# Optimization experiments

Hardware: AMD Instinct MI355X
Metric: run time of the kernel (lower is better)

Reference implementation:

```python
import jax, jax.numpy as jnp
import numpy as np
import math

B, S, D, H = 2, 2048, 1024, 16
DK = D // H


def setup_inputs() -> dict:
    key = jax.random.key(0)
    ks = jax.random.split(key, 11)
    s = 1.0 / math.sqrt(D)
    return {
        "q": jax.random.normal(ks[0], (B, S, D), jnp.float32),
        "k": jax.random.normal(ks[1], (B, S, D), jnp.float32),
        "v": jax.random.normal(ks[2], (B, S, D), jnp.float32),
        "Wq": jax.random.normal(ks[3], (D, D), jnp.float32) * s,
        "bq": jax.random.normal(ks[4], (D,), jnp.float32) * s,
        "Wk": jax.random.normal(ks[5], (D, D), jnp.float32) * s,
        "bk": jax.random.normal(ks[6], (D,), jnp.float32) * s,
        "Wv": jax.random.normal(ks[7], (D, D), jnp.float32) * s,
        "bv": jax.random.normal(ks[8], (D,), jnp.float32) * s,
        "Wo": jax.random.normal(ks[9], (D, D), jnp.float32) * s,
        "bo": jax.random.normal(ks[10], (D,), jnp.float32) * s,
    }


def reference(q, k, v, Wq, bq, Wk, bk, Wv, bv, Wo, bo):
    bs = q.shape[0]
    # linear projections, split heads: [B, H, S, DK]
    qh = (q @ Wq.T + bq).reshape(bs, -1, H, DK).transpose(0, 2, 1, 3)
    kh = (k @ Wk.T + bk).reshape(bs, -1, H, DK).transpose(0, 2, 1, 3)
    vh = (v @ Wv.T + bv).reshape(bs, -1, H, DK).transpose(0, 2, 1, 3)
    # scaled dot-product attention (dropout in eval mode -> identity)
    scores = jnp.einsum('bhqd,bhkd->bhqk', qh, kh) / math.sqrt(DK)
    attn = jax.nn.softmax(scores, axis=-1)
    out = jnp.einsum('bhqk,bhkd->bhqd', attn, vh)
    concat = out.transpose(0, 2, 1, 3).reshape(bs, -1, D)
    return concat @ Wo.T + bo
```

## Files before the change

kernel.cpp:

```cpp
#include <hip/hip_runtime.h>
#include <stdint.h>

#define DEV __device__ __forceinline__

typedef __bf16 bf16;
typedef __bf16 bf16x8 __attribute__((ext_vector_type(8)));
typedef unsigned short u16x8 __attribute__((ext_vector_type(8)));
typedef float f32x4 __attribute__((ext_vector_type(4)));
typedef uint32_t u32x4 __attribute__((ext_vector_type(4)));

static constexpr int S = 2048, D = 1024, NH = 16;
static constexpr float QSCALE = 0.125f * 1.44269504088896340736f;
static constexpr float DTHR = 8.0f;

union BU { u16x8 u; bf16x8 v; };
union PU { u32x4 u; bf16x8 v; };

DEV uint32_t pack2(float a, float b) {
  union { __bf16 h; uint16_t u; } x, y;
  x.h = (__bf16)a; y.h = (__bf16)b;
  return (uint32_t)x.u | ((uint32_t)y.u << 16);
}

struct CvtArgs { const float* s[7]; bf16* d[7]; };
__global__ __launch_bounds__(256) void cvt_all(CvtArgs a) {
  int blk = blockIdx.x, seg, rel;
  if (blk < 6144) { seg = blk >> 11; rel = blk & 2047; }
  else { int bb = blk - 6144; seg = 3 + (bb >> 9); rel = bb & 511; }
  int i = rel * 256 + threadIdx.x;
  const float4* p = (const float4*)a.s[seg] + (size_t)i * 2;
  float4 x = p[0], y = p[1];
  bf16x8 o;
  o[0] = (bf16)x.x; o[1] = (bf16)x.y; o[2] = (bf16)x.z; o[3] = (bf16)x.w;
  o[4] = (bf16)y.x; o[5] = (bf16)y.y; o[6] = (bf16)y.z; o[7] = (bf16)y.w;
  ((bf16x8*)a.d[seg])[i] = o;
}

DEV void async_copy16(bf16* lds_dst, const bf16* g_src) {
  __builtin_amdgcn_global_load_lds(
      (const __attribute__((address_space(1))) void*)(g_src),
      (__attribute__((address_space(3))) void*)(lds_dst),
      16, 0, 0);
}

struct GArgs {
  const bf16* A[3]; const bf16* W[3]; const float* bias[3];
  bf16* Cb[3]; float* Cf[3]; float scale[3];
};

template <bool OUT_F32>
__global__ __launch_bounds__(256, 2)
void gemm_multi(GArgs g) {
  constexpr int N = 1024, K = 1024;
  const int z = blockIdx.z;
  const bf16* A = g.A[z];
  const bf16* Bt = g.W[z];
  const float* bias = g.bias[z];
  const float scale = g.scale[z];

  __shared__ bf16 As[128 * 32];
  __shared__ bf16 Bs[64 * 32];
  const int t = threadIdx.x;
  const int w = t >> 6, l = t & 63;
  const int lr = l & 15, lg = l >> 4;
  const int m0 = blockIdx.y * 128, n0 = blockIdx.x * 64;

  f32x4 acc[2][4] = {};

  const int srow = t >> 2, scol = (t & 3) * 8;
  const bf16* Aptr = A + (size_t)(m0 + srow) * K + scol;
  const bf16* Bptr = Bt + (size_t)(n0 + srow) * K + scol;
  bf16* AsDst = &As[w * 512];
  bf16* BsDst = &Bs[w * 512];

  for (int k0 = 0; k0 < K; k0 += 32) {
    async_copy16(AsDst,        Aptr + k0);
    async_copy16(AsDst + 2048, Aptr + (size_t)64 * K + k0);
    async_copy16(BsDst,        Bptr + k0);
    __syncthreads();
    bf16x8 af[2], bfr[4];
#pragma unroll
    for (int i = 0; i < 2; i++)
      af[i] = *(const bf16x8*)&As[(w * 32 + i * 16 + lr) * 32 + lg * 8];
#pragma unroll
    for (int n = 0; n < 4; n++)
      bfr[n] = *(const bf16x8*)&Bs[(n * 16 + lr) * 32 + lg * 8];
#pragma unroll
    for (int mi = 0; mi < 2; mi++)
#pragma unroll
      for (int ni = 0; ni < 4; ni++)
        acc[mi][ni] = __builtin_amdgcn_mfma_f32_16x16x32_bf16(
            af[mi], bfr[ni], acc[mi][ni], 0, 0, 0);
    __syncthreads();
  }

#pragma unroll
  for (int mi = 0; mi < 2; mi++) {
#pragma unroll
    for (int ni = 0; ni < 4; ni++) {
      int col = n0 + ni * 16 + lr;
      float bv = bias[col];
#pragma unroll
      for (int r = 0; r < 4; r++) {
        int row = m0 + w * 32 + mi * 16 + lg * 4 + r;
        float v = (acc[mi][ni][r] + bv) * scale;
        if (OUT_F32) g.Cf[z][(size_t)row * N + col] = v;
        else         g.Cb[z][(size_t)row * N + col] = (bf16)v;
      }
    }
  }
}

__global__ __launch_bounds__(256, 2)
void attn_kernel(const bf16* __restrict__ Qp, const bf16* __restrict__ Kp,
                 const bf16* __restrict__ Vp, bf16* __restrict__ Oc) {
  __shared__ uint4 ldsu[2048];
  char* lds = (char*)ldsu;

  const int t = threadIdx.x, w = t >> 6, l = t & 63;
  const int lr = l & 15, lg = l >> 4;
  const int bh = blockIdx.y, b = bh >> 4, h = bh & 15;
  const int q0 = blockIdx.x * 128;
  const size_t base = (size_t)b * S * D + (size_t)h * 64;
  const size_t TILE = (size_t)64 * D;

  bf16x8 qf[2][2];
  {
    const bf16* qb = Qp + base + (size_t)(q0 + w * 32 + lr) * D + lg * 8;
#pragma unroll
    for (int qs = 0; qs < 2; qs++)
#pragma unroll
      for (int ks = 0; ks < 2; ks++)
        qf[qs][ks] = *(const bf16x8*)(qb + (size_t)qs * 16 * D + ks * 32);
  }

  f32x4 accO[2][4] = {};
  float mrun[2] = {-1e30f, -1e30f}, lsum[2] = {0.f, 0.f};

  const bf16* kptr[2];
#pragma unroll
  for (int c = 0; c < 2; c++) {
    int o = w * 2048 + c * 1024 + l * 16;
    int rho = o >> 7;
    int seg16 = ((o & 127) ^ ((rho & 7) << 4)) >> 4;
    int mm = rho >> 4;
    int srow = ((mm & 1) << 5) | (((rho >> 2) & 3) << 3) | ((mm >> 1) << 2) | (rho & 3);
    kptr[c] = Kp + base + (size_t)srow * D + seg16 * 8;
  }

  const int vu = t & 31, vc = t >> 5;
  const bf16* Vg = Vp + base + (size_t)(2 * vu) * D + vc * 8;
  int vwa[8];
#pragma unroll
  for (int j = 0; j < 8; j++)
    vwa[j] = 16384 + (((vc * 8 + j) * 128 + vu * 4) ^ (j << 4));

  const int rswz = (lr & 7) << 4;

  async_copy16((bf16*)(lds + w * 2048),        kptr[0]);
  async_copy16((bf16*)(lds + w * 2048 + 1024), kptr[1]);
  u16x8 va = *(const u16x8*)(Vg);
  u16x8 vb = *(const u16x8*)(Vg + D);
  __syncthreads();
  {
#pragma unroll
    for (int j = 0; j < 8; j++) {
      uint32_t dw = (uint32_t)va[j] | ((uint32_t)vb[j] << 16);
      *(uint32_t*)(lds + vwa[j]) = dw;
    }
  }
  va = *(const u16x8*)(Vg + TILE);
  vb = *(const u16x8*)(Vg + TILE + D);
  __syncthreads();

  const bf16* kp0 = kptr[0] + TILE;
  const bf16* kp1 = kptr[1] + TILE;
  const bf16* vg2 = Vg + 2 * TILE;

  for (int it = 0; it < 32; ++it) {
    const int cur = (it & 1) * 8192;
    const int nxt = ((it + 1) & 1) * 8192;
    const bool hasN = it < 31, hasN2 = it < 30;

    if (hasN) {
      async_copy16((bf16*)(lds + nxt + w * 2048),        kp0);
      async_copy16((bf16*)(lds + nxt + w * 2048 + 1024), kp1);
      kp0 += TILE; kp1 += TILE;
    }
    const bf16* pv = hasN2 ? vg2 : (Vp + base);
    u16x8 ta = *(const u16x8*)(pv);
    u16x8 tb = *(const u16x8*)(pv + D);
    vg2 += TILE;

    f32x4 sc[2][4] = {};
#pragma unroll
    for (int ks = 0; ks < 2; ks++) {
      BU kf[4];
#pragma unroll
      for (int m = 0; m < 4; m++)
        kf[m].u = *(const u16x8*)(lds + cur +
                   ((((m * 16 + lr) * 128) + ks * 64 + lg * 16) ^ rswz));
      __builtin_amdgcn_s_setprio(1);
#pragma unroll
      for (int m = 0; m < 4; m++)
#pragma unroll
        for (int qs = 0; qs < 2; qs++)
          sc[qs][m] = __builtin_amdgcn_mfma_f32_16x16x32_bf16(
              kf[m].v, qf[qs][ks], sc[qs][m], 0, 0, 0);
      __builtin_amdgcn_s_setprio(0);
    }

    float mx[2];
#pragma unroll
    for (int qs = 0; qs < 2; qs++) {
      float a0 = fmaxf(fmaxf(sc[qs][0][0], sc[qs][0][1]), fmaxf(sc[qs][0][2], sc[qs][0][3]));
      float a1 = fmaxf(fmaxf(sc[qs][1][0], sc[qs][1][1]), fmaxf(sc[qs][1][2], sc[qs][1][3]));
      float a2 = fmaxf(fmaxf(sc[qs][2][0], sc[qs][2][1]), fmaxf(sc[qs][2][2], sc[qs][2][3]));
      float a3 = fmaxf(fmaxf(sc[qs][3][0], sc[qs][3][1]), fmaxf(sc[qs][3][2], sc[qs][3][3]));
      mx[qs] = fmaxf(fmaxf(a0, a1), fmaxf(a2, a3));
    }
    bool stable = (mx[0] <= mrun[0] + DTHR) & (mx[1] <= mrun[1] + DTHR);
    if (!__all(stable)) {
      float alq[2];
#pragma unroll
      for (int qs = 0; qs < 2; qs++) {
        float m2 = fmaxf(mx[qs], __shfl_xor(mx[qs], 16));
        m2 = fmaxf(m2, __shfl_xor(m2, 32));
        float mn = fmaxf(mrun[qs], m2);
        float al = exp2f(mrun[qs] - mn);
        mrun[qs] = mn;
        lsum[qs] *= al;
        alq[qs] = al;
      }
#pragma unroll
      for (int qs = 0; qs < 2; qs++)
#pragma unroll
        for (int r = 0; r < 4; r++) {
          float a = __shfl(alq[qs], (lg << 4) | (lg * 4 + r));
#pragma unroll
          for (int n = 0; n < 4; n++) accO[qs][n][r] *= a;
        }
    }
    uint32_t pk[2][4][2];
#pragma unroll
    for (int qs = 0; qs < 2; qs++) {
      float s = 0.f;
#pragma unroll
      for (int m = 0; m < 4; m++) {
        float p0 = exp2f(sc[qs][m][0] - mrun[qs]);
        float p1 = exp2f(sc[qs][m][1] - mrun[qs]);
        float p2 = exp2f(sc[qs][m][2] - mrun[qs]);
        float p3 = exp2f(sc[qs][m][3] - mrun[qs]);
        s += (p0 + p1) + (p2 + p3);
        pk[qs][m][0] = pack2(p0, p1);
        pk[qs][m][1] = pack2(p2, p3);
      }
      lsum[qs] += s;
    }

    if (hasN) {
#pragma unroll
      for (int j = 0; j < 8; j++) {
        uint32_t dw = (uint32_t)va[j] | ((uint32_t)vb[j] << 16);
        *(uint32_t*)(lds + vwa[j] + nxt) = dw;
      }
    }

#pragma unroll
    for (int ks = 0; ks < 2; ks++) {
      PU pa[2];
#pragma unroll
      for (int qs = 0; qs < 2; qs++) {
        pa[qs].u[0] = pk[qs][ks][0];
        pa[qs].u[1] = pk[qs][ks][1];
        pa[qs].u[2] = pk[qs][2 + ks][0];
        pa[qs].u[3] = pk[qs][2 + ks][1];
      }
      BU vf[4];
#pragma unroll
      for (int n = 0; n < 4; n++)
        vf[n].u = *(const u16x8*)(lds + 16384 + cur +
                   ((((n * 16 + lr) * 128) + ks * 64 + lg * 16) ^ rswz));
      __builtin_amdgcn_s_setprio(1);
#pragma unroll
      for (int n = 0; n < 4; n++)
#pragma unroll
        for (int qs = 0; qs < 2; qs++)
          accO[qs][n] = __builtin_amdgcn_mfma_f32_16x16x32_bf16(
              pa[qs].v, vf[n].v, accO[qs][n], 0, 0, 0);
      __builtin_amdgcn_s_setprio(0);
    }

    va = ta; vb = tb;
    __syncthreads();
  }

#pragma unroll
  for (int qs = 0; qs < 2; qs++) {
    lsum[qs] += __shfl_xor(lsum[qs], 16);
    lsum[qs] += __shfl_xor(lsum[qs], 32);
  }
#pragma unroll
  for (int qs = 0; qs < 2; qs++)
#pragma unroll
    for (int r = 0; r < 4; r++) {
      float lv = __shfl(lsum[qs], (lg << 4) | (lg * 4 + r));
      float rl = 1.0f / lv;
      int row = q0 + w * 32 + qs * 16 + lg * 4 + r;
      bf16* orow = Oc + base + (size_t)row * D;
#pragma unroll
      for (int n = 0; n < 4; n++) orow[n * 16 + lr] = (bf16)(accO[qs][n][r] * rl);
    }
}

extern "C" void kernel_launch(void* const* d_in, const int* in_sizes, int n_in,
                              void* d_out, int out_size, void* d_ws, size_t ws_size,
                              hipStream_t stream) {
  const float* q  = (const float*)d_in[0];
  const float* k  = (const float*)d_in[1];
  const float* v  = (const float*)d_in[2];
  const float* Wq = (const float*)d_in[3];
  const float* bq = (const float*)d_in[4];
  const float* Wk = (const float*)d_in[5];
  const float* bk = (const float*)d_in[6];
  const float* Wv = (const float*)d_in[7];
  const float* bv = (const float*)d_in[8];
  const float* Wo = (const float*)d_in[9];
  const float* bo = (const float*)d_in[10];
  float* out = (float*)d_out;

  const int BS = 2 * S;
  const size_t SZ_T = (size_t)BS * D * 2;
  const size_t SZ_W = (size_t)D * D * 2;

  char* ws = (char*)d_ws;
  bf16* qb  = (bf16*)(ws);
  bf16* kb  = (bf16*)(ws + SZ_T);
  bf16* vb  = (bf16*)(ws + 2 * SZ_T);
  bf16* Wqb = (bf16*)(ws + 3 * SZ_T);
  bf16* Wkb = (bf16*)(ws + 3 * SZ_T + SZ_W);
  bf16* Wvb = (bf16*)(ws + 3 * SZ_T + 2 * SZ_W);
  bf16* Wob = (bf16*)(ws + 3 * SZ_T + 3 * SZ_W);
  bf16* Qh  = (bf16*)(ws + 3 * SZ_T + 4 * SZ_W);
  bf16* Kh  = (bf16*)(ws + 4 * SZ_T + 4 * SZ_W);
  bf16* Vh  = (bf16*)(ws + 5 * SZ_T + 4 * SZ_W);
  bf16* Oc  = qb;

  CvtArgs ca;
  ca.s[0] = q;  ca.d[0] = qb;
  ca.s[1] = k;  ca.d[1] = kb;
  ca.s[2] = v;  ca.d[2] = vb;
  ca.s[3] = Wq; ca.d[3] = Wqb;
  ca.s[4] = Wk; ca.d[4] = Wkb;
  ca.s[5] = Wv; ca.d[5] = Wvb;
  ca.s[6] = Wo; ca.d[6] = Wob;
  cvt_all<<<dim3(8192), 256, 0, stream>>>(ca);

  GArgs gp = {};
  gp.A[0] = qb; gp.W[0] = Wqb; gp.bias[0] = bq; gp.Cb[0] = Qh; gp.scale[0] = QSCALE;
  gp.A[1] = kb; gp.W[1] = Wkb; gp.bias[1] = bk; gp.Cb[1] = Kh; gp.scale[1] = 1.0f;
  gp.A[2] = vb; gp.W[2] = Wvb; gp.bias[2] = bv; gp.Cb[2] = Vh; gp.scale[2] = 1.0f;
  gemm_multi<false><<<dim3(D / 64, BS / 128, 3), 256, 0, stream>>>(gp);

  attn_kernel<<<dim3(S / 128, 2 * NH), 256, 0, stream>>>(Qh, Kh, Vh, Oc);

  GArgs go = {};
  go.A[0] = Oc; go.W[0] = Wob; go.bias[0] = bo; go.Cf[0] = out; go.scale[0] = 1.0f;
  gemm_multi<true><<<dim3(D / 64, BS / 128, 1), 256, 0, stream>>>(go);
}
```

Before: 253.5 us.

## Use 128x128 QKV GEMM tiles and 8-wave attention blocks with lazy-max softmax

The QKV projection GEMM moves to 128x128 output tiles with a 2x2 wave grid, so each loaded tile is reused more. The output projection gets its own specialised fp32 kernel. The attention kernel runs 512 threads with one 16-row query strip per wave, and softmax changes to exponentiate first against a fixed running max (starting at 4) and rescale only when a row sum exceeds a threshold. This cuts the per-tile max reduction, but it relies on scores staying bounded to avoid overflow, and the smaller per-wave work lowers K/V reuse per MFMA.

```diff
diff --git a/kernel.cpp b/kernel.cpp
--- a/kernel.cpp
+++ b/kernel.cpp
@@ -6,12 +6,13 @@
 typedef __bf16 bf16;
 typedef __bf16 bf16x8 __attribute__((ext_vector_type(8)));
 typedef unsigned short u16x8 __attribute__((ext_vector_type(8)));
+typedef unsigned short u16x4 __attribute__((ext_vector_type(4)));
 typedef float f32x4 __attribute__((ext_vector_type(4)));
 typedef uint32_t u32x4 __attribute__((ext_vector_type(4)));
 
 static constexpr int S = 2048, D = 1024, NH = 16;
 static constexpr float QSCALE = 0.125f * 1.44269504088896340736f;
-static constexpr float DTHR = 8.0f;
+static constexpr float STHR = 4096.0f;
 
 union BU { u16x8 u; bf16x8 v; };
 union PU { u32x4 u; bf16x8 v; };
@@ -45,12 +46,11 @@
 
 struct GArgs {
   const bf16* A[3]; const bf16* W[3]; const float* bias[3];
-  bf16* Cb[3]; float* Cf[3]; float scale[3];
+  bf16* Cb[3]; float scale[3];
 };
 
-template <bool OUT_F32>
 __global__ __launch_bounds__(256, 2)
-void gemm_multi(GArgs g) {
+void gemm128(GArgs g) {
   constexpr int N = 1024, K = 1024;
   const int z = blockIdx.z;
   const bf16* A = g.A[z];
@@ -59,6 +59,63 @@
   const float scale = g.scale[z];
 
   __shared__ bf16 As[128 * 32];
+  __shared__ bf16 Bs[128 * 32];
+  const int t = threadIdx.x;
+  const int w = t >> 6, l = t & 63;
+  const int wr = w >> 1, wc = w & 1;
+  const int lr = l & 15, lg = l >> 4;
+  const int m0 = blockIdx.y * 128, n0 = blockIdx.x * 128;
+
+  f32x4 acc[4][4] = {};
+
+  const int srow = t >> 2, scol = (t & 3) * 8;
+  const bf16* Aptr = A + (size_t)(m0 + srow) * K + scol;
+  const bf16* Bptr = Bt + (size_t)(n0 + srow) * K + scol;
+  bf16* AsDst = &As[w * 512];
+  bf16* BsDst = &Bs[w * 512];
+
+  for (int k0 = 0; k0 < K; k0 += 32) {
+    async_copy16(AsDst,        Aptr + k0);
+    async_copy16(AsDst + 2048, Aptr + (size_t)64 * K + k0);
+    async_copy16(BsDst,        Bptr + k0);
+    async_copy16(BsDst + 2048, Bptr + (size_t)64 * K + k0);
+    __syncthreads();
+    bf16x8 af[4], bfr[4];
+#pragma unroll
+    for (int i = 0; i < 4; i++)
+      af[i] = *(const bf16x8*)&As[(wr * 64 + i * 16 + lr) * 32 + lg * 8];
+#pragma unroll
+    for (int i = 0; i < 4; i++)
+      bfr[i] = *(const bf16x8*)&Bs[(wc * 64 + i * 16 + lr) * 32 + lg * 8];
+#pragma unroll
+    for (int mi = 0; mi < 4; mi++)
+#pragma unroll
+      for (int ni = 0; ni < 4; ni++)
+        acc[mi][ni] = __builtin_amdgcn_mfma_f32_16x16x32_bf16(
+            af[mi], bfr[ni], acc[mi][ni], 0, 0, 0);
+    __syncthreads();
+  }
+
+#pragma unroll
+  for (int mi = 0; mi < 4; mi++) {
+#pragma unroll
+    for (int ni = 0; ni < 4; ni++) {
+      int col = n0 + wc * 64 + ni * 16 + lr;
+      float bv = bias[col];
+#pragma unroll
+      for (int r = 0; r < 4; r++) {
+        int row = m0 + wr * 64 + mi * 16 + lg * 4 + r;
+        g.Cb[z][(size_t)row * N + col] = (bf16)((acc[mi][ni][r] + bv) * scale);
+      }
+    }
+  }
+}
+
+__global__ __launch_bounds__(256, 2)
+void gemm64out(const bf16* __restrict__ A, const bf16* __restrict__ Bt,
+               const float* __restrict__ bias, float* __restrict__ Cf) {
+  constexpr int N = 1024, K = 1024;
+  __shared__ bf16 As[128 * 32];
   __shared__ bf16 Bs[64 * 32];
   const int t = threadIdx.x;
   const int w = t >> 6, l = t & 63;
@@ -103,15 +160,13 @@
 #pragma unroll
       for (int r = 0; r < 4; r++) {
         int row = m0 + w * 32 + mi * 16 + lg * 4 + r;
-        float v = (acc[mi][ni][r] + bv) * scale;
-        if (OUT_F32) g.Cf[z][(size_t)row * N + col] = v;
-        else         g.Cb[z][(size_t)row * N + col] = (bf16)v;
+        Cf[(size_t)row * N + col] = acc[mi][ni][r] + bv;
       }
     }
   }
 }
 
-__global__ __launch_bounds__(256, 2)
+__global__ __launch_bounds__(512, 4)
 void attn_kernel(const bf16* __restrict__ Qp, const bf16* __restrict__ Kp,
                  const bf16* __restrict__ Vp, bf16* __restrict__ Oc) {
   __shared__ uint4 ldsu[2048];
@@ -124,75 +179,68 @@
   const size_t base = (size_t)b * S * D + (size_t)h * 64;
   const size_t TILE = (size_t)64 * D;
 
-  bf16x8 qf[2][2];
+  bf16x8 qf[2];
   {
-    const bf16* qb = Qp + base + (size_t)(q0 + w * 32 + lr) * D + lg * 8;
-#pragma unroll
-    for (int qs = 0; qs < 2; qs++)
-#pragma unroll
-      for (int ks = 0; ks < 2; ks++)
-        qf[qs][ks] = *(const bf16x8*)(qb + (size_t)qs * 16 * D + ks * 32);
-  }
-
-  f32x4 accO[2][4] = {};
-  float mrun[2] = {-1e30f, -1e30f}, lsum[2] = {0.f, 0.f};
-
-  const bf16* kptr[2];
-#pragma unroll
-  for (int c = 0; c < 2; c++) {
-    int o = w * 2048 + c * 1024 + l * 16;
+    const bf16* qrow = Qp + base + (size_t)(q0 + w * 16 + lr) * D + lg * 8;
+    qf[0] = *(const bf16x8*)(qrow);
+    qf[1] = *(const bf16x8*)(qrow + 32);
+  }
+
+  f32x4 accO[4] = {};
+  float mrun = 4.0f, lsum = 0.f;
+
+  const bf16* kptr;
+  {
+    int o = t * 16;
     int rho = o >> 7;
     int seg16 = ((o & 127) ^ ((rho & 7) << 4)) >> 4;
     int mm = rho >> 4;
     int srow = ((mm & 1) << 5) | (((rho >> 2) & 3) << 3) | ((mm >> 1) << 2) | (rho & 3);
-    kptr[c] = Kp + base + (size_t)srow * D + seg16 * 8;
-  }
-
-  const int vu = t & 31, vc = t >> 5;
-  const bf16* Vg = Vp + base + (size_t)(2 * vu) * D + vc * 8;
-  int vwa[8];
-#pragma unroll
-  for (int j = 0; j < 8; j++)
-    vwa[j] = 16384 + (((vc * 8 + j) * 128 + vu * 4) ^ (j << 4));
+    kptr = Kp + base + (size_t)srow * D + seg16 * 8;
+  }
+  bf16* kdst = (bf16*)(lds + w * 1024);
+
+  const int vu = t & 31, vcc = t >> 5;
+  const bf16* Vg = Vp + base + (size_t)(2 * vu) * D + vcc * 4;
+  int vwa[4];
+#pragma unroll
+  for (int j = 0; j < 4; j++) {
+    int d = vcc * 4 + j;
+    vwa[j] = 16384 + ((d * 128 + vu * 4) ^ ((d & 7) << 4));
+  }
 
   const int rswz = (lr & 7) << 4;
 
-  async_copy16((bf16*)(lds + w * 2048),        kptr[0]);
-  async_copy16((bf16*)(lds + w * 2048 + 1024), kptr[1]);
-  u16x8 va = *(const u16x8*)(Vg);
-  u16x8 vb = *(const u16x8*)(Vg + D);
+  async_copy16(kdst, kptr);
+  u16x4 va = *(const u16x4*)(Vg);
+  u16x4 vb = *(const u16x4*)(Vg + D);
   __syncthreads();
-  {
-#pragma unroll
-    for (int j = 0; j < 8; j++) {
-      uint32_t dw = (uint32_t)va[j] | ((uint32_t)vb[j] << 16);
-      *(uint32_t*)(lds + vwa[j]) = dw;
-    }
-  }
-  va = *(const u16x8*)(Vg + TILE);
-  vb = *(const u16x8*)(Vg + TILE + D);
+#pragma unroll
+  for (int j = 0; j < 4; j++)
+    *(uint32_t*)(lds + vwa[j]) = (uint32_t)va[j] | ((uint32_t)vb[j] << 16);
+  va = *(const u16x4*)(Vg + TILE);
+  vb = *(const u16x4*)(Vg + TILE + D);
   __syncthreads();
 
-  const bf16* kp0 = kptr[0] + TILE;
-  const bf16* kp1 = kptr[1] + TILE;
+  const bf16* kp1 = kptr + TILE;
   const bf16* vg2 = Vg + 2 * TILE;
 
+#pragma unroll 2
   for (int it = 0; it < 32; ++it) {
     const int cur = (it & 1) * 8192;
     const int nxt = ((it + 1) & 1) * 8192;
     const bool hasN = it < 31, hasN2 = it < 30;
 
     if (hasN) {
-      async_copy16((bf16*)(lds + nxt + w * 2048),        kp0);
-      async_copy16((bf16*)(lds + nxt + w * 2048 + 1024), kp1);
-      kp0 += TILE; kp1 += TILE;
+      async_copy16((bf16*)(lds + nxt + w * 1024), kp1);
+      kp1 += TILE;
     }
     const bf16* pv = hasN2 ? vg2 : (Vp + base);
-    u16x8 ta = *(const u16x8*)(pv);
-    u16x8 tb = *(const u16x8*)(pv + D);
+    u16x4 ta = *(const u16x4*)(pv);
+    u16x4 tb = *(const u16x4*)(pv + D);
     vg2 += TILE;
 
-    f32x4 sc[2][4] = {};
+    f32x4 sc[4] = {};
 #pragma unroll
     for (int ks = 0; ks < 2; ks++) {
       BU kf[4];
@@ -203,79 +251,65 @@
       __builtin_amdgcn_s_setprio(1);
 #pragma unroll
       for (int m = 0; m < 4; m++)
-#pragma unroll
-        for (int qs = 0; qs < 2; qs++)
-          sc[qs][m] = __builtin_amdgcn_mfma_f32_16x16x32_bf16(
-              kf[m].v, qf[qs][ks], sc[qs][m], 0, 0, 0);
+        sc[m] = __builtin_amdgcn_mfma_f32_16x16x32_bf16(
+            kf[m].v, qf[ks], sc[m], 0, 0, 0);
       __builtin_amdgcn_s_setprio(0);
     }
 
-    float mx[2];
-#pragma unroll
-    for (int qs = 0; qs < 2; qs++) {
-      float a0 = fmaxf(fmaxf(sc[qs][0][0], sc[qs][0][1]), fmaxf(sc[qs][0][2], sc[qs][0][3]));
-      float a1 = fmaxf(fmaxf(sc[qs][1][0], sc[qs][1][1]), fmaxf(sc[qs][1][2], sc[qs][1][3]));
-      float a2 = fmaxf(fmaxf(sc[qs][2][0], sc[qs][2][1]), fmaxf(sc[qs][2][2], sc[qs][2][3]));
-      float a3 = fmaxf(fmaxf(sc[qs][3][0], sc[qs][3][1]), fmaxf(sc[qs][3][2], sc[qs][3][3]));
-      mx[qs] = fmaxf(fmaxf(a0, a1), fmaxf(a2, a3));
-    }
-    bool stable = (mx[0] <= mrun[0] + DTHR) & (mx[1] <= mrun[1] + DTHR);
-    if (!__all(stable)) {
-      float alq[2];
-#pragma unroll
-      for (int qs = 0; qs < 2; qs++) {
-        float m2 = fmaxf(mx[qs], __shfl_xor(mx[qs], 16));
-        m2 = fmaxf(m2, __shfl_xor(m2, 32));
-        float mn = fmaxf(mrun[qs], m2);
-        float al = exp2f(mrun[qs] - mn);
-        mrun[qs] = mn;
-        lsum[qs] *= al;
-        alq[qs] = al;
+    float s = 0.f;
+#pragma unroll
+    for (int m = 0; m < 4; m++) {
+      sc[m][0] = exp2f(sc[m][0] - mrun);
+      sc[m][1] = exp2f(sc[m][1] - mrun);
+      sc[m][2] = exp2f(sc[m][2] - mrun);
+      sc[m][3] = exp2f(sc[m][3] - mrun);
+      s += (sc[m][0] + sc[m][1]) + (sc[m][2] + sc[m][3]);
+    }
+    if (!__all(s <= STHR)) {
+      float pm = sc[0][0];
+#pragma unroll
+      for (int m = 0; m < 4; m++)
+#pragma unroll
+        for (int r = 0; r < 4; r++) pm = fmaxf(pm, sc[m][r]);
+      pm = fmaxf(pm, __shfl_xor(pm, 16));
+      pm = fmaxf(pm, __shfl_xor(pm, 32));
+      float mn = fmaxf(mrun + __log2f(pm), mrun);
+      float f = exp2f(mrun - mn);
+      mrun = mn;
+      s *= f;
+      lsum *= f;
+#pragma unroll
+      for (int m = 0; m < 4; m++)
+#pragma unroll
+        for (int r = 0; r < 4; r++) sc[m][r] *= f;
+#pragma unroll
+      for (int r = 0; r < 4; r++) {
+        float a = __shfl(f, (lg << 4) | (lg * 4 + r));
+#pragma unroll
+        for (int n = 0; n < 4; n++) accO[n][r] *= a;
       }
-#pragma unroll
-      for (int qs = 0; qs < 2; qs++)
-#pragma unroll
-        for (int r = 0; r < 4; r++) {
-          float a = __shfl(alq[qs], (lg << 4) | (lg * 4 + r));
-#pragma unroll
-          for (int n = 0; n < 4; n++) accO[qs][n][r] *= a;
-        }
-    }
-    uint32_t pk[2][4][2];
-#pragma unroll
-    for (int qs = 0; qs < 2; qs++) {
-      float s = 0.f;
-#pragma unroll
-      for (int m = 0; m < 4; m++) {
-        float p0 = exp2f(sc[qs][m][0] - mrun[qs]);
-        float p1 = exp2f(sc[qs][m][1] - mrun[qs]);
-        float p2 = exp2f(sc[qs][m][2] - mrun[qs]);
-        float p3 = exp2f(sc[qs][m][3] - mrun[qs]);
-        s += (p0 + p1) + (p2 + p3);
-        pk[qs][m][0] = pack2(p0, p1);
-        pk[qs][m][1] = pack2(p2, p3);
-      }
-      lsum[qs] += s;
+    }
+    lsum += s;
+    uint32_t pk[4][2];
+#pragma unroll
+    for (int m = 0; m < 4; m++) {
+      pk[m][0] = pack2(sc[m][0], sc[m][1]);
+      pk[m][1] = pack2(sc[m][2], sc[m][3]);
     }
 
     if (hasN) {
 #pragma unroll
-      for (int j = 0; j < 8; j++) {
-        uint32_t dw = (uint32_t)va[j] | ((uint32_t)vb[j] << 16);
-        *(uint32_t*)(lds + vwa[j] + nxt) = dw;
-      }
+      for (int j = 0; j < 4; j++)
+        *(uint32_t*)(lds + vwa[j] + nxt) = (uint32_t)va[j] | ((uint32_t)vb[j] << 16);
     }
 
 #pragma unroll
     for (int ks = 0; ks < 2; ks++) {
-      PU pa[2];
-#pragma unroll
-      for (int qs = 0; qs < 2; qs++) {
-        pa[qs].u[0] = pk[qs][ks][0];
-        pa[qs].u[1] = pk[qs][ks][1];
-        pa[qs].u[2] = pk[qs][2 + ks][0];
-        pa[qs].u[3] = pk[qs][2 + ks][1];
-      }
+      PU pa;
+      pa.u[0] = pk[ks][0];
+      pa.u[1] = pk[ks][1];
+      pa.u[2] = pk[2 + ks][0];
+      pa.u[3] = pk[2 + ks][1];
       BU vf[4];
 #pragma unroll
       for (int n = 0; n < 4; n++)
@@ -284,10 +318,8 @@
       __builtin_amdgcn_s_setprio(1);
 #pragma unroll
       for (int n = 0; n < 4; n++)
-#pragma unroll
-        for (int qs = 0; qs < 2; qs++)
-          accO[qs][n] = __builtin_amdgcn_mfma_f32_16x16x32_bf16(
-              pa[qs].v, vf[n].v, accO[qs][n], 0, 0, 0);
+        accO[n] = __builtin_amdgcn_mfma_f32_16x16x32_bf16(
+            pa.v, vf[n].v, accO[n], 0, 0, 0);
       __builtin_amdgcn_s_setprio(0);
     }
 
@@ -295,22 +327,17 @@
     __syncthreads();
   }
 
-#pragma unroll
-  for (int qs = 0; qs < 2; qs++) {
-    lsum[qs] += __shfl_xor(lsum[qs], 16);
-    lsum[qs] += __shfl_xor(lsum[qs], 32);
-  }
-#pragma unroll
-  for (int qs = 0; qs < 2; qs++)
-#pragma unroll
-    for (int r = 0; r < 4; r++) {
-      float lv = __shfl(lsum[qs], (lg << 4) | (lg * 4 + r));
-      float rl = 1.0f / lv;
-      int row = q0 + w * 32 + qs * 16 + lg * 4 + r;
-      bf16* orow = Oc + base + (size_t)row * D;
-#pragma unroll
-      for (int n = 0; n < 4; n++) orow[n * 16 + lr] = (bf16)(accO[qs][n][r] * rl);
-    }
+  lsum += __shfl_xor(lsum, 16);
+  lsum += __shfl_xor(lsum, 32);
+#pragma unroll
+  for (int r = 0; r < 4; r++) {
+    float lv = __shfl(lsum, (lg << 4) | (lg * 4 + r));
+    float rl = 1.0f / lv;
+    int row = q0 + w * 16 + lg * 4 + r;
+    bf16* orow = Oc + base + (size_t)row * D;
+#pragma unroll
+    for (int n = 0; n < 4; n++) orow[n * 16 + lr] = (bf16)(accO[n][r] * rl);
+  }
 }
 
 extern "C" void kernel_launch(void* const* d_in, const int* in_sizes, int n_in,
@@ -360,11 +387,9 @@
   gp.A[0] = qb; gp.W[0] = Wqb; gp.bias[0] = bq; gp.Cb[0] = Qh; gp.scale[0] = QSCALE;
   gp.A[1] = kb; gp.W[1] = Wkb; gp.bias[1] = bk; gp.Cb[1] = Kh; gp.scale[1] = 1.0f;
   gp.A[2] = vb; gp.W[2] = Wvb; gp.bias[2] = bv; gp.Cb[2] = Vh; gp.scale[2] = 1.0f;
-  gemm_multi<false><<<dim3(D / 64, BS / 128, 3), 256, 0, stream>>>(gp);
-
-  attn_kernel<<<dim3(S / 128, 2 * NH), 256, 0, stream>>>(Qh, Kh, Vh, Oc);
-
-  GArgs go = {};
-  go.A[0] = Oc; go.W[0] = Wob; go.bias[0] = bo; go.Cf[0] = out; go.scale[0] = 1.0f;
-  gemm_multi<true><<<dim3(D / 64, BS / 128, 1), 256, 0, stream>>>(go);
-}
+  gemm128<<<dim3(D / 128, BS / 128, 3), 256, 0, stream>>>(gp);
+
+  attn_kernel<<<dim3(S / 128, 2 * NH), 512, 0, stream>>>(Qh, Kh, Vh, Oc);
+
+  gemm64out<<<dim3(D / 64, BS / 128), 256, 0, stream>>>(Oc, Wob, bo, out);
+}
```

Result: faster. 237.0 us (-6.5%).
